# Performance work log

Hardware: AMD Instinct MI355X
Metric: run time of the kernel (lower is better)

Reference implementation:

```python
import jax, jax.numpy as jnp
import numpy as np

B, T, CIN = 8, 4096, 512
GROUP, ENTRY = 2, 320
COUT = 512
D = COUT // GROUP  # per-group codebook dim = 256


def setup_inputs() -> dict:
    key = jax.random.key(0)
    k_x, k_w, k_cb, k_g = jax.random.split(key, 4)
    x = jax.random.normal(k_x, (B, T, CIN), dtype=jnp.float32)
    # weight_proj: Linear(in_channel, group*entry)
    Wp = jax.random.normal(k_w, (GROUP * ENTRY, CIN), dtype=jnp.float32) * (1.0 / np.sqrt(CIN))
    bp = jnp.zeros((GROUP * ENTRY,), dtype=jnp.float32)
    # stacked codebooks: [group, entry, out_channel//group]
    codebooks = jax.random.normal(k_cb, (GROUP, ENTRY, D), dtype=jnp.float32)
    # pre-sampled gumbel noise (torch gumbel_softmax samples this internally)
    gumbel = jax.random.gumbel(k_g, (B, T, GROUP * ENTRY), dtype=jnp.float32)
    return {"x": x, "Wp": Wp, "bp": bp, "codebooks": codebooks, "gumbel": gumbel}


def reference(x, Wp, bp, codebooks, gumbel):
    # weight_proj
    logits = jnp.einsum('btc,ec->bte', x, Wp) + bp          # [B,T,group*entry]
    # gumbel_softmax(tau=1, hard=False, dim=-1): softmax over full group*entry axis
    y = jax.nn.softmax(logits + gumbel, axis=-1)            # [B,T,group*entry]
    # chunk into groups -> contiguous reshape matches torch.chunk
    yg = y.reshape(B, T, GROUP, ENTRY)                      # [B,T,G,E]
    # per-group matmul against codebook weights, then concat over groups
    out = jnp.einsum('btge,ged->btgd', yg, codebooks)       # [B,T,G,D]
    return out.reshape(B, T, GROUP * D)                     # [B,T,out_channel]
```

## Files before the change

### kernel.cpp

```cpp
#include <hip/hip_runtime.h>
#include <hip/hip_bf16.h>
#include <stdint.h>

#define BT     32768
#define CIN    512
#define NE     640
#define ENTRY  320
#define DD     256
#define MROWS  64
#define TPB    512

using bf16x8 = __attribute__((ext_vector_type(8))) short;
using f32x4  = __attribute__((ext_vector_type(4))) float;
using u16x8  = __attribute__((ext_vector_type(8))) unsigned short;

#define X_OFF   0
#define X_STRB  1040
#define Y_OFF   66560
#define Y_STRB  1296
#define Y_STRE  648
#define S_OFF   149504
#define SMEM_BYTES 149760

__device__ __forceinline__ unsigned short f2b(float f) {
    union { float f; uint32_t u; } v; v.f = f;
    uint32_t u = v.u;
    return (unsigned short)((u + 0x7FFFu + ((u >> 16) & 1u)) >> 16);
}

__global__ void prep_kernel(const float* __restrict__ Wp, const float* __restrict__ cb,
                            unsigned short* __restrict__ WpB, unsigned short* __restrict__ cbT) {
    int i = blockIdx.x * blockDim.x + threadIdx.x;
    if (i < NE * CIN) {
        WpB[i] = f2b(Wp[i]);
    } else {
        int o = i - NE * CIN;
        if (o < 2 * ENTRY * DD) {
            int g = o / (DD * ENTRY);
            int r = o - g * (DD * ENTRY);
            int d = r / ENTRY;
            int e = r - d * ENTRY;
            cbT[o] = f2b(cb[(g * ENTRY + e) * DD + d]);
        }
    }
}

__global__ __launch_bounds__(TPB, 2) void fused_kernel(
    const float* __restrict__ x, const float* __restrict__ bp,
    const float* __restrict__ gum, const unsigned short* __restrict__ WpB,
    const unsigned short* __restrict__ cbT, float* __restrict__ out) {

    extern __shared__ char smem[];
    unsigned short* yS = (unsigned short*)(smem + Y_OFF);
    float*          sS = (float*)(smem + S_OFF);

    const int tid = threadIdx.x;
    const int w  = tid >> 6;
    const int l  = tid & 63;
    const int q  = l >> 4;
    const int ln = l & 15;
    const int rowbase = blockIdx.x * MROWS;

    if (tid < MROWS) sS[tid] = 0.0f;

#pragma unroll
    for (int i = 0; i < 8; ++i) {
        int c   = tid + i * TPB;
        int row = c >> 6;
        int c8  = c & 63;
        const float* p = x + (size_t)(rowbase + row) * CIN + c8 * 8;
        float4 a = *(const float4*)p;
        float4 b = *(const float4*)(p + 4);
        u16x8 hv;
        hv[0] = f2b(a.x); hv[1] = f2b(a.y); hv[2] = f2b(a.z); hv[3] = f2b(a.w);
        hv[4] = f2b(b.x); hv[5] = f2b(b.y); hv[6] = f2b(b.z); hv[7] = f2b(b.w);
        *(u16x8*)(smem + X_OFF + row * X_STRB + c8 * 16) = hv;
    }

    const float* gbase = gum + (size_t)rowbase * NE + w * 80 + ln;
    float gv[5];
#pragma unroll
    for (int j = 0; j < 5; ++j) gv[j] = gbase[(size_t)(q * 4) * NE + j * 16];

    f32x4 acc1[4][5];
    const f32x4 fz = {0.f, 0.f, 0.f, 0.f};
#pragma unroll
    for (int rt = 0; rt < 4; ++rt)
#pragma unroll
        for (int j = 0; j < 5; ++j) acc1[rt][j] = fz;

    const unsigned short* bp1 = WpB + (size_t)(w * 80 + ln) * CIN + q * 8;
    bf16x8 bc[5], bn[5];
#pragma unroll
    for (int j = 0; j < 5; ++j) bc[j] = *(const bf16x8*)(bp1 + (size_t)j * 16 * CIN);

    __syncthreads();

#pragma unroll 1
    for (int ks = 0; ks < 16; ++ks) {
        const int k0 = ks * 32;
        if (ks < 15) {
#pragma unroll
            for (int j = 0; j < 5; ++j)
                bn[j] = *(const bf16x8*)(bp1 + (size_t)j * 16 * CIN + k0 + 32);
        }
        bf16x8 af[4];
#pragma unroll
        for (int rt = 0; rt < 4; ++rt)
            af[rt] = *(const bf16x8*)(smem + X_OFF + (rt * 16 + ln) * X_STRB + (k0 + q * 8) * 2);
#pragma unroll
        for (int j = 0; j < 5; ++j)
#pragma unroll
            for (int rt = 0; rt < 4; ++rt)
                acc1[rt][j] = __builtin_amdgcn_mfma_f32_16x16x32_bf16(af[rt], bc[j], acc1[rt][j], 0, 0, 0);
        if (ks < 15) {
#pragma unroll
            for (int j = 0; j < 5; ++j) bc[j] = bn[j];
        }
    }

    float bpv[5];
#pragma unroll
    for (int j = 0; j < 5; ++j) bpv[j] = bp[w * 80 + j * 16 + ln];

#pragma unroll
    for (int ri = 0; ri < 16; ++ri) {
        float gn[5];
        if (ri < 15) {
            int nrow = ((ri + 1) >> 2) * 16 + q * 4 + ((ri + 1) & 3);
            const float* pn = gbase + (size_t)nrow * NE;
#pragma unroll
            for (int j = 0; j < 5; ++j) gn[j] = pn[j * 16];
        }
        const int rt = ri >> 2, r = ri & 3;
        const int row = rt * 16 + q * 4 + r;
        float p = 0.f;
#pragma unroll
        for (int j = 0; j < 5; ++j) {
            float v = acc1[rt][j][r] + bpv[j] + gv[j];
            float e = __expf(v);
            yS[row * Y_STRE + w * 80 + j * 16 + ln] = f2b(e);
            p += e;
        }
        p += __shfl_xor(p, 1);
        p += __shfl_xor(p, 2);
        p += __shfl_xor(p, 4);
        p += __shfl_xor(p, 8);
        if (ln == 0) atomicAdd(&sS[row], p);
#pragma unroll
        for (int j = 0; j < 5; ++j) gv[j] = gn[j];
    }

    const int g   = w >> 2;
    const int nbp = (w & 3) * 64;

    f32x4 acc2[4][4];
#pragma unroll
    for (int rt = 0; rt < 4; ++rt)
#pragma unroll
        for (int ct = 0; ct < 4; ++ct) acc2[rt][ct] = fz;

    const unsigned short* cp = cbT + (size_t)(g * DD + nbp + ln) * ENTRY + q * 8;
    bf16x8 cc[4], cn[4];
#pragma unroll
    for (int ct = 0; ct < 4; ++ct) cc[ct] = *(const bf16x8*)(cp + (size_t)ct * 16 * ENTRY);

    __syncthreads();

#pragma unroll 1
    for (int ks = 0; ks < 10; ++ks) {
        const int k0 = ks * 32;
        if (ks < 9) {
#pragma unroll
            for (int ct = 0; ct < 4; ++ct)
                cn[ct] = *(const bf16x8*)(cp + (size_t)ct * 16 * ENTRY + k0 + 32);
        }
        bf16x8 af2[4];
#pragma unroll
        for (int rt = 0; rt < 4; ++rt)
            af2[rt] = *(const bf16x8*)(smem + Y_OFF + (rt * 16 + ln) * Y_STRB + (g * ENTRY + k0 + q * 8) * 2);
#pragma unroll
        for (int ct = 0; ct < 4; ++ct)
#pragma unroll
            for (int rt = 0; rt < 4; ++rt)
                acc2[rt][ct] = __builtin_amdgcn_mfma_f32_16x16x32_bf16(af2[rt], cc[ct], acc2[rt][ct], 0, 0, 0);
        if (ks < 9) {
#pragma unroll
            for (int ct = 0; ct < 4; ++ct) cc[ct] = cn[ct];
        }
    }

#pragma unroll
    for (int rt = 0; rt < 4; ++rt) {
#pragma unroll
        for (int r = 0; r < 4; ++r) {
            const int row = rt * 16 + q * 4 + r;
            const float inv = 1.0f / sS[row];
            float* op = out + (size_t)(rowbase + row) * 512 + g * DD + nbp + ln;
#pragma unroll
            for (int ct = 0; ct < 4; ++ct)
                op[ct * 16] = acc2[rt][ct][r] * inv;
        }
    }
}

extern "C" void kernel_launch(void* const* d_in, const int* in_sizes, int n_in,
                              void* d_out, int out_size, void* d_ws, size_t ws_size,
                              hipStream_t stream) {
    const float* x   = (const float*)d_in[0];
    const float* Wp  = (const float*)d_in[1];
    const float* bp  = (const float*)d_in[2];
    const float* cb  = (const float*)d_in[3];
    const float* gum = (const float*)d_in[4];
    float* out = (float*)d_out;

    unsigned short* WpB = (unsigned short*)d_ws;
    unsigned short* cbT = WpB + NE * CIN;

    int prep_total = NE * CIN + 2 * ENTRY * DD;
    prep_kernel<<<(prep_total + 255) / 256, 256, 0, stream>>>(Wp, cb, WpB, cbT);

    fused_kernel<<<dim3(BT / MROWS), dim3(TPB), SMEM_BYTES, stream>>>(x, bp, gum, WpB, cbT, out);
}
```

Baseline: 251.1 us.

## Stage gumbel noise into LDS via async global_load_lds during GEMM1

Gumbel noise is now prefetched asynchronously into shared memory with global_load_lds, issued before the first GEMM loop. Previously it was loaded per thread from global memory with strided scalar reads during the softmax phase. Shared memory is reorganised so the gumbel staging buffers alias the X tile and the second Y half. The softmax is processed in 16-row chunks with extra barriers so buffers can be reused. This hides gumbel load latency behind MFMA work and coalesces the reads, at the cost of more __syncthreads and a more intricate buffer-aliasing schedule.

New measurement: 254.2 us. Within noise of the previous version (+1.2%).

```diff
diff --git a/kernel.cpp b/kernel.cpp
--- a/kernel.cpp
+++ b/kernel.cpp
@@ -14,18 +14,55 @@
 using f32x4  = __attribute__((ext_vector_type(4))) float;
 using u16x8  = __attribute__((ext_vector_type(8))) unsigned short;
 
-#define X_OFF   0
-#define X_STRB  1040
-#define Y_OFF   66560
-#define Y_STRB  1296
-#define Y_STRE  648
-#define S_OFF   149504
-#define SMEM_BYTES 149760
+#define X_STRB   1040
+#define Y_STRB   1296
+#define GUMA_OFF 66560
+#define Y2_OFF   107520
+#define S_OFF    148992
+#define SMEM_BYTES 149248
 
 __device__ __forceinline__ unsigned short f2b(float f) {
     union { float f; uint32_t u; } v; v.f = f;
     uint32_t u = v.u;
     return (unsigned short)((u + 0x7FFFu + ((u >> 16) & 1u)) >> 16);
+}
+
+__device__ __forceinline__ void gl2lds16(const void* g, void* l) {
+    __builtin_amdgcn_global_load_lds((const __attribute__((address_space(1))) void*)g,
+                                     (__attribute__((address_space(3))) void*)l, 16, 0, 0);
+}
+
+__device__ __forceinline__ void stage_gum_chunk(const float* gsrc, char* lbuf, int w, int l) {
+#pragma unroll
+    for (int ii = 0; ii < 5; ++ii) {
+        const int i = w + ii * 8;
+        gl2lds16((const char*)gsrc + i * 1024 + l * 16, lbuf + i * 1024);
+    }
+}
+
+__device__ __forceinline__ void proc_chunk(const float* gl, char* ybase, float* sS,
+                                           const f32x4 (&ac)[5], const float (&bpv)[5],
+                                           int srow, int w, int q, int ln) {
+#pragma unroll
+    for (int r = 0; r < 4; ++r) {
+        const int rl = q * 4 + r;
+        float g5[5];
+#pragma unroll
+        for (int j = 0; j < 5; ++j) g5[j] = gl[rl * 640 + w * 80 + j * 16 + ln];
+        float p = 0.f;
+#pragma unroll
+        for (int j = 0; j < 5; ++j) {
+            float v = ac[j][r] + bpv[j] + g5[j];
+            float e = __expf(v);
+            *(unsigned short*)(ybase + rl * Y_STRB + (w * 80 + j * 16 + ln) * 2) = f2b(e);
+            p += e;
+        }
+        p += __shfl_xor(p, 1);
+        p += __shfl_xor(p, 2);
+        p += __shfl_xor(p, 4);
+        p += __shfl_xor(p, 8);
+        if (ln == 0) atomicAdd(&sS[srow + rl], p);
+    }
 }
 
 __global__ void prep_kernel(const float* __restrict__ Wp, const float* __restrict__ cb,
@@ -51,8 +88,7 @@
     const unsigned short* __restrict__ cbT, float* __restrict__ out) {
 
     extern __shared__ char smem[];
-    unsigned short* yS = (unsigned short*)(smem + Y_OFF);
-    float*          sS = (float*)(smem + S_OFF);
+    float* sS = (float*)(smem + S_OFF);
 
     const int tid = threadIdx.x;
     const int w  = tid >> 6;
@@ -74,13 +110,8 @@
         u16x8 hv;
         hv[0] = f2b(a.x); hv[1] = f2b(a.y); hv[2] = f2b(a.z); hv[3] = f2b(a.w);
         hv[4] = f2b(b.x); hv[5] = f2b(b.y); hv[6] = f2b(b.z); hv[7] = f2b(b.w);
-        *(u16x8*)(smem + X_OFF + row * X_STRB + c8 * 16) = hv;
-    }
-
-    const float* gbase = gum + (size_t)rowbase * NE + w * 80 + ln;
-    float gv[5];
-#pragma unroll
-    for (int j = 0; j < 5; ++j) gv[j] = gbase[(size_t)(q * 4) * NE + j * 16];
+        *(u16x8*)(smem + row * X_STRB + c8 * 16) = hv;
+    }
 
     f32x4 acc1[4][5];
     const f32x4 fz = {0.f, 0.f, 0.f, 0.f};
@@ -95,6 +126,9 @@
     for (int j = 0; j < 5; ++j) bc[j] = *(const bf16x8*)(bp1 + (size_t)j * 16 * CIN);
 
     __syncthreads();
+
+    stage_gum_chunk(gum + (size_t)(rowbase +  0) * NE, smem + GUMA_OFF, w, l);
+    stage_gum_chunk(gum + (size_t)(rowbase + 16) * NE, smem + Y2_OFF,   w, l);
 
 #pragma unroll 1
     for (int ks = 0; ks < 16; ++ks) {
@@ -107,63 +141,46 @@
         bf16x8 af[4];
 #pragma unroll
         for (int rt = 0; rt < 4; ++rt)
-            af[rt] = *(const bf16x8*)(smem + X_OFF + (rt * 16 + ln) * X_STRB + (k0 + q * 8) * 2);
+            af[rt] = *(const bf16x8*)(smem + (rt * 16 + ln) * X_STRB + (k0 + q * 8) * 2);
 #pragma unroll
         for (int j = 0; j < 5; ++j)
 #pragma unroll
             for (int rt = 0; rt < 4; ++rt)
                 acc1[rt][j] = __builtin_amdgcn_mfma_f32_16x16x32_bf16(af[rt], bc[j], acc1[rt][j], 0, 0, 0);
-        if (ks < 15) {
-#pragma unroll
-            for (int j = 0; j < 5; ++j) bc[j] = bn[j];
-        }
+#pragma unroll
+        for (int j = 0; j < 5; ++j) bc[j] = bn[j];
     }
 
     float bpv[5];
 #pragma unroll
     for (int j = 0; j < 5; ++j) bpv[j] = bp[w * 80 + j * 16 + ln];
 
-#pragma unroll
-    for (int ri = 0; ri < 16; ++ri) {
-        float gn[5];
-        if (ri < 15) {
-            int nrow = ((ri + 1) >> 2) * 16 + q * 4 + ((ri + 1) & 3);
-            const float* pn = gbase + (size_t)nrow * NE;
-#pragma unroll
-            for (int j = 0; j < 5; ++j) gn[j] = pn[j * 16];
-        }
-        const int rt = ri >> 2, r = ri & 3;
-        const int row = rt * 16 + q * 4 + r;
-        float p = 0.f;
-#pragma unroll
-        for (int j = 0; j < 5; ++j) {
-            float v = acc1[rt][j][r] + bpv[j] + gv[j];
-            float e = __expf(v);
-            yS[row * Y_STRE + w * 80 + j * 16 + ln] = f2b(e);
-            p += e;
-        }
-        p += __shfl_xor(p, 1);
-        p += __shfl_xor(p, 2);
-        p += __shfl_xor(p, 4);
-        p += __shfl_xor(p, 8);
-        if (ln == 0) atomicAdd(&sS[row], p);
-#pragma unroll
-        for (int j = 0; j < 5; ++j) gv[j] = gn[j];
-    }
+    __syncthreads();
+
+    proc_chunk((const float*)(smem + GUMA_OFF), smem, sS, acc1[0], bpv, 0, w, q, ln);
+    __syncthreads();
+    stage_gum_chunk(gum + (size_t)(rowbase + 32) * NE, smem + GUMA_OFF, w, l);
+    proc_chunk((const float*)(smem + Y2_OFF), smem + 16 * Y_STRB, sS, acc1[1], bpv, 16, w, q, ln);
+    __syncthreads();
+    proc_chunk((const float*)(smem + GUMA_OFF), smem + Y2_OFF, sS, acc1[2], bpv, 32, w, q, ln);
+    __syncthreads();
+    stage_gum_chunk(gum + (size_t)(rowbase + 48) * NE, smem + GUMA_OFF, w, l);
 
     const int g   = w >> 2;
     const int nbp = (w & 3) * 64;
-
-    f32x4 acc2[4][4];
-#pragma unroll
-    for (int rt = 0; rt < 4; ++rt)
-#pragma unroll
-        for (int ct = 0; ct < 4; ++ct) acc2[rt][ct] = fz;
-
     const unsigned short* cp = cbT + (size_t)(g * DD + nbp + ln) * ENTRY + q * 8;
     bf16x8 cc[4], cn[4];
 #pragma unroll
     for (int ct = 0; ct < 4; ++ct) cc[ct] = *(const bf16x8*)(cp + (size_t)ct * 16 * ENTRY);
+
+    __syncthreads();
+    proc_chunk((const float*)(smem + GUMA_OFF), smem + Y2_OFF + 16 * Y_STRB, sS, acc1[3], bpv, 48, w, q, ln);
+
+    f32x4 acc2[4][4];
+#pragma unroll
+    for (int rt = 0; rt < 4; ++rt)
+#pragma unroll
+        for (int ct = 0; ct < 4; ++ct) acc2[rt][ct] = fz;
 
     __syncthreads();
 
@@ -175,19 +192,19 @@
             for (int ct = 0; ct < 4; ++ct)
                 cn[ct] = *(const bf16x8*)(cp + (size_t)ct * 16 * ENTRY + k0 + 32);
         }
+        const int coff = (g * ENTRY + k0 + q * 8) * 2;
         bf16x8 af2[4];
-#pragma unroll
-        for (int rt = 0; rt < 4; ++rt)
-            af2[rt] = *(const bf16x8*)(smem + Y_OFF + (rt * 16 + ln) * Y_STRB + (g * ENTRY + k0 + q * 8) * 2);
+        af2[0] = *(const bf16x8*)(smem + (ln)      * Y_STRB + coff);
+        af2[1] = *(const bf16x8*)(smem + (16 + ln) * Y_STRB + coff);
+        af2[2] = *(const bf16x8*)(smem + Y2_OFF + (ln)      * Y_STRB + coff);
+        af2[3] = *(const bf16x8*)(smem + Y2_OFF + (16 + ln) * Y_STRB + coff);
 #pragma unroll
         for (int ct = 0; ct < 4; ++ct)
 #pragma unroll
             for (int rt = 0; rt < 4; ++rt)
                 acc2[rt][ct] = __builtin_amdgcn_mfma_f32_16x16x32_bf16(af2[rt], cc[ct], acc2[rt][ct], 0, 0, 0);
-        if (ks < 9) {
-#pragma unroll
-            for (int ct = 0; ct < 4; ++ct) cc[ct] = cn[ct];
-        }
+#pragma unroll
+        for (int ct = 0; ct < 4; ++ct) cc[ct] = cn[ct];
     }
 
 #pragma unroll
```
